# Kernel optimization log

Measured on AMD Instinct MI355X. Metric: run time of the kernel, lower is better.

The kernel has to match this reference:

```python
import jax, jax.numpy as jnp
from jax import lax
import numpy as np

SUB_SAMPLE = 16
NMS_THRESH = 0.7
N_PRE_NMS = 2000
N_POST_NMS = 300
MIN_SIZE = 16.0
SCALE = 1.0
NEG_INF = -1e9


def _anchor_base(base=16.0, ratios=(0.5, 1.0, 2.0), scales=(8.0, 16.0, 32.0)):
    r = np.asarray(ratios, np.float32)[:, None]
    s = np.asarray(scales, np.float32)[None, :]
    h = base * s * np.sqrt(r)
    w = base * s * np.sqrt(1.0 / r)
    ctr = base / 2.0
    ab = np.stack([ctr - h / 2, ctr - w / 2, ctr + h / 2, ctr + w / 2], axis=-1)
    return ab.reshape(-1, 4).astype(np.float32)  # [9,4] (y1,x1,y2,x2)


def _decode(anchors, locs):
    # anchors/locs: [K,4]; loc2bbox
    ah = anchors[:, 2] - anchors[:, 0]
    aw = anchors[:, 3] - anchors[:, 1]
    acy = anchors[:, 0] + 0.5 * ah
    acx = anchors[:, 1] + 0.5 * aw
    dy, dx, dh, dw = locs[:, 0], locs[:, 1], locs[:, 2], locs[:, 3]
    cy = dy * ah + acy
    cx = dx * aw + acx
    h = jnp.exp(dh) * ah
    w = jnp.exp(dw) * aw
    return jnp.stack([cy - 0.5 * h, cx - 0.5 * w, cy + 0.5 * h, cx + 0.5 * w], axis=-1)


def _pairwise_iou(b):
    # b: [P,4] y1x1y2x2
    tl = jnp.maximum(b[:, None, :2], b[None, :, :2])
    br = jnp.minimum(b[:, None, 2:], b[None, :, 2:])
    wh = jnp.clip(br - tl, 0.0)
    inter = wh[..., 0] * wh[..., 1]
    area = (b[:, 2] - b[:, 0]) * (b[:, 3] - b[:, 1])
    return inter / (area[:, None] + area[None, :] - inter + 1e-9)


def _propose(locs_i, fg_i, anchors, img_h, img_w):
    boxes = _decode(anchors, locs_i)
    boxes = jnp.stack([
        jnp.clip(boxes[:, 0], 0.0, img_h), jnp.clip(boxes[:, 1], 0.0, img_w),
        jnp.clip(boxes[:, 2], 0.0, img_h), jnp.clip(boxes[:, 3], 0.0, img_w)], axis=-1)
    hs = boxes[:, 2] - boxes[:, 0]
    ws = boxes[:, 3] - boxes[:, 1]
    ok = (hs >= MIN_SIZE * SCALE) & (ws >= MIN_SIZE * SCALE)
    sc = jnp.where(ok, fg_i, NEG_INF)
    top_sc, order = lax.top_k(sc, N_PRE_NMS)  # sorted desc by score
    b = boxes[order]
    iou = _pairwise_iou(b)
    idx = jnp.arange(N_PRE_NMS)
    sup = (iou > NMS_THRESH) & (idx[None, :] > idx[:, None])  # only suppress lower-scored
    keep0 = top_sc > NEG_INF / 2  # drop min-size-filtered padding

    def body(i, keep):
        return jnp.where(keep[i], keep & ~sup[i], keep)

    keep = lax.fori_loop(0, N_PRE_NMS, body, keep0)
    prio = jnp.where(keep, idx, N_PRE_NMS)
    sel = jnp.argsort(prio)[:N_POST_NMS]  # kept boxes first, score order preserved
    valid = keep[sel]
    rois = jnp.where(valid[:, None], b[sel], 0.0)
    return rois, valid


def setup_inputs() -> dict:
    key = jax.random.key(0)
    ks = jax.random.split(key, 6)
    N, C, Hf, Wf = 8, 512, 64, 64
    std = 0.01  # normal_init(0, 0.01)
    return {
        "x": jax.random.normal(ks[0], (N, C, Hf, Wf), jnp.float32),
        "conv1_w": jax.random.normal(ks[1], (512, 512, 3, 3), jnp.float32) * std,
        "conv1_b": jnp.zeros((512,), jnp.float32),
        "score_w": jax.random.normal(ks[2], (18, 512, 1, 1), jnp.float32) * std,
        "score_b": jnp.zeros((18,), jnp.float32),
        "loc_w": jax.random.normal(ks[3], (36, 512, 1, 1), jnp.float32) * std,
        "loc_b": jnp.zeros((36,), jnp.float32),
        "img_h": 1024,
        "img_w": 1024,
    }


def reference(x, conv1_w, conv1_b, score_w, score_b, loc_w, loc_b, img_h, img_w):
    N, _, Hf, Wf = x.shape
    ab = jnp.asarray(_anchor_base())
    A = ab.shape[0]
    sy = jnp.arange(Hf, dtype=jnp.float32) * SUB_SAMPLE
    sx = jnp.arange(Wf, dtype=jnp.float32) * SUB_SAMPLE
    Y, X = jnp.meshgrid(sy, sx, indexing='ij')
    shifts = jnp.stack([Y, X, Y, X], axis=-1).reshape(-1, 4)
    anchors = (shifts[:, None, :] + ab[None, :, :]).reshape(-1, 4)  # [H*W*A,4]

    hidden = jax.nn.relu(
        lax.conv_general_dilated(x, conv1_w, (1, 1), 'SAME',
                                 dimension_numbers=('NCHW', 'OIHW', 'NCHW'))
        + conv1_b[None, :, None, None])
    scores = jnp.einsum('nchw,oc->nhwo', hidden, score_w[:, :, 0, 0]) + score_b  # [N,H,W,2A]
    locs = jnp.einsum('nchw,oc->nhwo', hidden, loc_w[:, :, 0, 0]) + loc_b        # [N,H,W,4A]

    rpn_locs = locs.reshape(N, -1, 4)
    rpn_scores = scores.reshape(N, -1, 2)
    soft = jax.nn.softmax(scores.reshape(N, Hf, Wf, A, 2), axis=-1)
    rpn_fg = soft[..., 1].reshape(N, -1)

    fh = jnp.float32(img_h)
    fw = jnp.float32(img_w)
    rois, valid = jax.vmap(lambda l, s: _propose(l, s, anchors, fh, fw))(rpn_locs, rpn_fg)
    roi_indices = jnp.repeat(jnp.arange(N, dtype=jnp.int32), N_POST_NMS)
    return rpn_locs, rpn_scores, rois.reshape(-1, 4), roi_indices, anchors
```

## Files before the change

### kernel.cpp

```cpp
#include <hip/hip_runtime.h>
#include <math.h>

typedef unsigned int u32;
typedef unsigned long long u64;

#define NIMG 8
#define CIN 512
#define COUT 512
#define HF 64
#define WF 64
#define NPOS 4096
#define NANCH 36864
#define NPRE 2000
#define NPOST 300
#define SUPW 32

#define OUT_LOCS   0
#define OUT_SCORES 1179648
#define OUT_ROIS   1769472
#define OUT_ROIIDX 1779072
#define OUT_ANCH   1781472

__device__ __forceinline__ u32 fkey(float f) {
  u32 s = __float_as_uint(f);
  return (s & 0x80000000u) ? ~s : (s | 0x80000000u);
}
__device__ __forceinline__ float unkey(u32 u) {
  u32 s = (u & 0x80000000u) ? (u ^ 0x80000000u) : ~u;
  return __uint_as_float(s);
}
__device__ __forceinline__ void anchor_at(int hq, int wq, int a,
                                          float& a0, float& a1, float& a2, float& a3) {
  const float ratios[3] = {0.5f, 1.0f, 2.0f};
  const float scales[3] = {8.0f, 16.0f, 32.0f};
  float r = ratios[a / 3];
  float s = scales[a % 3];
  float hh = __fmul_rn(__fmul_rn(16.0f, s), sqrtf(r));
  float ww = __fmul_rn(__fmul_rn(16.0f, s), sqrtf(1.0f / r));
  float ab0 = __fsub_rn(8.0f, __fmul_rn(0.5f, hh));
  float ab1 = __fsub_rn(8.0f, __fmul_rn(0.5f, ww));
  float ab2 = __fadd_rn(8.0f, __fmul_rn(0.5f, hh));
  float ab3 = __fadd_rn(8.0f, __fmul_rn(0.5f, ww));
  float y = (float)(hq * 16);
  float x = (float)(wq * 16);
  a0 = __fadd_rn(y, ab0);
  a1 = __fadd_rn(x, ab1);
  a2 = __fadd_rn(y, ab2);
  a3 = __fadd_rn(x, ab3);
}
__device__ __forceinline__ u64 shfl_u64(u64 v, int src) {
  u32 lo = (u32)v, hi = (u32)(v >> 32);
  lo = __shfl(lo, src, 64);
  hi = __shfl(hi, src, 64);
  return ((u64)hi << 32) | (u64)lo;
}

__global__ __launch_bounds__(256) void k_transpose_w(const float* __restrict__ w,
                                                     float* __restrict__ wt) {
  int o = blockIdx.x * 256 + threadIdx.x;
  if (o >= COUT * CIN * 9) return;
  int co = o & 511;
  int r = o >> 9;
  int tap = r % 9;
  int ci = r / 9;
  wt[o] = w[((size_t)co * CIN + ci) * 9 + tap];
}

__global__ __launch_bounds__(256) void k_prep_small(const float* __restrict__ sw,
                                                    const float* __restrict__ lw,
                                                    float* __restrict__ wt54,
                                                    float* __restrict__ out) {
  int i = blockIdx.x * 256 + threadIdx.x;
  if (i < 512 * 56) {
    int c = i / 56, o = i % 56;
    float v = 0.0f;
    if (o < 18) v = sw[o * 512 + c];
    else if (o < 54) v = lw[(o - 18) * 512 + c];
    wt54[i] = v;
  }
  if (i < NANCH) {
    int pos = i / 9, a = i % 9;
    float a0, a1, a2, a3;
    anchor_at(pos >> 6, pos & 63, a, a0, a1, a2, a3);
    float* dst = out + OUT_ANCH + (size_t)i * 4;
    dst[0] = a0; dst[1] = a1; dst[2] = a2; dst[3] = a3;
  }
  if (i < NIMG * NPOST) out[OUT_ROIIDX + i] = (float)(i / NPOST);
}

#define CC 8
__global__ __launch_bounds__(256) void k_conv3x3(const float* __restrict__ x,
                                                 const float* __restrict__ wt,
                                                 const float* __restrict__ bias,
                                                 float* __restrict__ hidden) {
  __shared__ float in_lds[4][CC][68];
  __shared__ float w_lds[CC][9][64];
  const int tid = threadIdx.x;
  const int h0 = blockIdx.x * 2;
  const int n = blockIdx.y;
  const int co_t = blockIdx.z * 64;
  const int wq = tid & 15, cq = tid >> 4;
  const int w0 = wq * 4;
  const float* xn = x + (size_t)n * CIN * NPOS;
  float acc[2][4][4] = {};
  for (int ci0 = 0; ci0 < CIN; ci0 += CC) {
    for (int idx = tid; idx < 4 * CC * 66; idx += 256) {
      int wp = idx % 66;
      int r = idx / 66;
      int cc = r % CC, rr = r / CC;
      int hh = h0 - 1 + rr, ww = wp - 1;
      float v = 0.0f;
      if (hh >= 0 && hh < HF && ww >= 0 && ww < WF)
        v = xn[(size_t)(ci0 + cc) * NPOS + hh * WF + ww];
      in_lds[rr][cc][wp] = v;
    }
    for (int idx = tid; idx < CC * 9 * 64; idx += 256) {
      int co = idx & 63;
      int r = idx >> 6;
      int tap = r % 9, cc = r / 9;
      w_lds[cc][tap][co] = wt[((size_t)(ci0 + cc) * 9 + tap) * COUT + co_t + co];
    }
    __syncthreads();
    for (int cc = 0; cc < CC; ++cc) {
      float a[4][6];
      #pragma unroll
      for (int r = 0; r < 4; ++r)
        #pragma unroll
        for (int k = 0; k < 6; ++k)
          a[r][k] = in_lds[r][cc][w0 + k];
      #pragma unroll
      for (int kh = 0; kh < 3; ++kh) {
        #pragma unroll
        for (int kw = 0; kw < 3; ++kw) {
          const float4 b4 = *(const float4*)&w_lds[cc][kh * 3 + kw][cq * 4];
          #pragma unroll
          for (int r = 0; r < 2; ++r) {
            #pragma unroll
            for (int w = 0; w < 4; ++w) {
              float av = a[r + kh][w + kw];
              acc[r][w][0] = fmaf(av, b4.x, acc[r][w][0]);
              acc[r][w][1] = fmaf(av, b4.y, acc[r][w][1]);
              acc[r][w][2] = fmaf(av, b4.z, acc[r][w][2]);
              acc[r][w][3] = fmaf(av, b4.w, acc[r][w][3]);
            }
          }
        }
      }
    }
    __syncthreads();
  }
  #pragma unroll
  for (int c = 0; c < 4; ++c) {
    float b = bias[co_t + cq * 4 + c];
    #pragma unroll
    for (int r = 0; r < 2; ++r) {
      float4 v;
      v.x = fmaxf(acc[r][0][c] + b, 0.0f);
      v.y = fmaxf(acc[r][1][c] + b, 0.0f);
      v.z = fmaxf(acc[r][2][c] + b, 0.0f);
      v.w = fmaxf(acc[r][3][c] + b, 0.0f);
      *(float4*)&hidden[(((size_t)n * COUT + co_t + cq * 4 + c) * HF + h0 + r) * WF + w0] = v;
    }
  }
}

__global__ __launch_bounds__(256) void k_heads(const float* __restrict__ hidden,
                                               const float* __restrict__ wt54,
                                               const float* __restrict__ sb,
                                               const float* __restrict__ lb,
                                               const int* __restrict__ ihp,
                                               const int* __restrict__ iwp,
                                               float* __restrict__ out,
                                               float4* __restrict__ boxes_all,
                                               u64* __restrict__ k64) {
  const int n = blockIdx.y;
  const int hw = blockIdx.x * 256 + threadIdx.x;
  const float* hid = hidden + (size_t)n * CIN * NPOS + hw;
  float acc[54];
  #pragma unroll
  for (int o = 0; o < 54; ++o) acc[o] = 0.0f;
  #pragma unroll 4
  for (int c = 0; c < CIN; ++c) {
    float hv = hid[(size_t)c * NPOS];
    const float* wrow = wt54 + c * 56;
    #pragma unroll
    for (int o = 0; o < 54; ++o) acc[o] = fmaf(hv, wrow[o], acc[o]);
  }
  float sc18[18];
  #pragma unroll
  for (int o = 0; o < 18; ++o) sc18[o] = __fadd_rn(acc[o], sb[o]);
  float lc36[36];
  #pragma unroll
  for (int o = 0; o < 36; ++o) lc36[o] = __fadd_rn(acc[18 + o], lb[o]);
  {
    float* dst = out + OUT_SCORES + ((size_t)n * NPOS + hw) * 18;
    #pragma unroll
    for (int q = 0; q < 9; ++q) *(float2*)&dst[q * 2] = make_float2(sc18[2 * q], sc18[2 * q + 1]);
  }
  {
    float* dst = out + OUT_LOCS + ((size_t)n * NPOS + hw) * 36;
    #pragma unroll
    for (int q = 0; q < 9; ++q)
      *(float4*)&dst[q * 4] = make_float4(lc36[4 * q], lc36[4 * q + 1], lc36[4 * q + 2], lc36[4 * q + 3]);
  }
  const float fh = (float)ihp[0];
  const float fw = (float)iwp[0];
  const int hq = hw >> 6, wq2 = hw & 63;
  #pragma unroll
  for (int a = 0; a < 9; ++a) {
    float a0, a1, a2, a3;
    anchor_at(hq, wq2, a, a0, a1, a2, a3);
    float ah = __fsub_rn(a2, a0), aw = __fsub_rn(a3, a1);
    float acy = __fadd_rn(a0, __fmul_rn(0.5f, ah));
    float acx = __fadd_rn(a1, __fmul_rn(0.5f, aw));
    float dy = lc36[4 * a], dx = lc36[4 * a + 1], dh = lc36[4 * a + 2], dw = lc36[4 * a + 3];
    float cy = __fadd_rn(__fmul_rn(dy, ah), acy);
    float cx = __fadd_rn(__fmul_rn(dx, aw), acx);
    float hh = __fmul_rn(expf(dh), ah);
    float ww = __fmul_rn(expf(dw), aw);
    float y1 = __fsub_rn(cy, __fmul_rn(0.5f, hh));
    float x1 = __fsub_rn(cx, __fmul_rn(0.5f, ww));
    float y2 = __fadd_rn(cy, __fmul_rn(0.5f, hh));
    float x2 = __fadd_rn(cx, __fmul_rn(0.5f, ww));
    y1 = fminf(fmaxf(y1, 0.0f), fh);
    y2 = fminf(fmaxf(y2, 0.0f), fh);
    x1 = fminf(fmaxf(x1, 0.0f), fw);
    x2 = fminf(fmaxf(x2, 0.0f), fw);
    float hs = __fsub_rn(y2, y1), wsz = __fsub_rn(x2, x1);
    bool ok = (hs >= 16.0f) && (wsz >= 16.0f);
    float l0 = sc18[2 * a], l1 = sc18[2 * a + 1];
    float m = fmaxf(l0, l1);
    float e0 = expf(__fsub_rn(l0, m));
    float e1 = expf(__fsub_rn(l1, m));
    float fg = __fdiv_rn(e1, __fadd_rn(e0, e1));
    float sc = ok ? fg : -1000000000.0f;
    int idx = hw * 9 + a;
    boxes_all[(size_t)n * NANCH + idx] = make_float4(y1, x1, y2, x2);
    k64[(size_t)n * NANCH + idx] = ((u64)(~fkey(sc)) << 16) | (u32)idx;
  }
}

__global__ __launch_bounds__(1024) void k_topk(const u64* __restrict__ k64_all,
                                               const float4* __restrict__ boxes_all,
                                               float4* __restrict__ boxes_sorted,
                                               float* __restrict__ sc_sorted) {
  const int b = blockIdx.x;
  const int tid = threadIdx.x;
  const u64* kb = k64_all + (size_t)b * NANCH;
  __shared__ u32 hist[4096];
  __shared__ u32 coarse[1024];
  __shared__ u64 sortbuf[2048];
  __shared__ u32 sh_bucket, sh_before, sh_cnt;
  u64 prefix = 0ull;
  u32 rank = NPRE;
  for (int pass = 0; pass < 4; ++pass) {
    const int shift = 36 - 12 * pass;
    for (int i = tid; i < 4096; i += 1024) hist[i] = 0;
    __syncthreads();
    for (int i = tid; i < NANCH; i += 1024) {
      u64 k = kb[i];
      if ((k >> (shift + 12)) == prefix)
        atomicAdd(&hist[(u32)((k >> shift) & 4095ull)], 1u);
    }
    __syncthreads();
    u32 s = hist[4 * tid] + hist[4 * tid + 1] + hist[4 * tid + 2] + hist[4 * tid + 3];
    coarse[tid] = s;
    __syncthreads();
    for (int off = 1; off < 1024; off <<= 1) {
      u32 v = (tid >= off) ? coarse[tid - off] : 0u;
      __syncthreads();
      coarse[tid] += v;
      __syncthreads();
    }
    u32 lo = (tid == 0) ? 0u : coarse[tid - 1];
    u32 hi = coarse[tid];
    if (lo < rank && rank <= hi) {
      u32 c = lo;
      #pragma unroll
      for (int q = 0; q < 4; ++q) {
        u32 nb = c + hist[4 * tid + q];
        if (c < rank && rank <= nb) { sh_bucket = 4 * tid + q; sh_before = c; break; }
        c = nb;
      }
    }
    __syncthreads();
    prefix = (prefix << 12) | (u64)sh_bucket;
    rank -= sh_before;
    __syncthreads();
  }
  const u64 Kstar = prefix;
  if (tid == 0) sh_cnt = 0;
  __syncthreads();
  for (int i = tid; i < NANCH; i += 1024) {
    u64 k = kb[i];
    if (k <= Kstar) {
      u32 p = atomicAdd(&sh_cnt, 1u);
      if (p < 2048) sortbuf[p] = k;
    }
  }
  __syncthreads();
  u32 cnt = sh_cnt;
  for (int i = tid; i < 2048; i += 1024)
    if (i >= (int)cnt) sortbuf[i] = ~0ull;
  __syncthreads();
  for (int kk = 2; kk <= 2048; kk <<= 1) {
    for (int j = kk >> 1; j > 0; j >>= 1) {
      int i1 = 2 * j * (tid / j) + (tid % j);
      int i2 = i1 + j;
      bool up = ((i1 & kk) == 0);
      u64 va = sortbuf[i1], vb = sortbuf[i2];
      if ((va > vb) == up) { sortbuf[i1] = vb; sortbuf[i2] = va; }
      __syncthreads();
    }
  }
  for (int i = tid; i < NPRE; i += 1024) {
    u64 k = sortbuf[i];
    u32 idx = (u32)(k & 0xFFFFull);
    boxes_sorted[(size_t)b * NPRE + i] = boxes_all[(size_t)b * NANCH + idx];
    sc_sorted[(size_t)b * NPRE + i] = unkey(~(u32)(k >> 16));
  }
}

__global__ __launch_bounds__(64) void k_supmask(const float4* __restrict__ boxes_sorted,
                                                u64* __restrict__ sup) {
  const int b = blockIdx.z;
  const int i = blockIdx.x * 64 + threadIdx.x;
  const int j0 = blockIdx.y * 64;
  __shared__ float4 bj[64];
  int jg = j0 + threadIdx.x;
  bj[threadIdx.x] = (jg < NPRE) ? boxes_sorted[(size_t)b * NPRE + jg] : make_float4(0, 0, 0, 0);
  __syncthreads();
  if (i >= NPRE) return;
  float4 bi = boxes_sorted[(size_t)b * NPRE + i];
  float ai = __fmul_rn(__fsub_rn(bi.z, bi.x), __fsub_rn(bi.w, bi.y));
  u64 m = 0;
  for (int q = 0; q < 64; ++q) {
    int j = j0 + q;
    float4 bb = bj[q];
    float ty = fmaxf(bi.x, bb.x);
    float tx = fmaxf(bi.y, bb.y);
    float by = fminf(bi.z, bb.z);
    float bx = fminf(bi.w, bb.w);
    float ih2 = fmaxf(__fsub_rn(by, ty), 0.0f);
    float iw2 = fmaxf(__fsub_rn(bx, tx), 0.0f);
    float inter = __fmul_rn(ih2, iw2);
    float aj = __fmul_rn(__fsub_rn(bb.z, bb.x), __fsub_rn(bb.w, bb.y));
    float den = __fadd_rn(__fsub_rn(__fadd_rn(ai, aj), inter), 1e-9f);
    float iou = __fdiv_rn(inter, den);
    if (iou > 0.7f && j > i && j < NPRE) m |= (1ull << q);
  }
  sup[((size_t)b * NPRE + i) * SUPW + blockIdx.y] = m;
}

__global__ __launch_bounds__(64) void k_nms(const u64* __restrict__ sup,
                                            const float* __restrict__ sc_sorted,
                                            const float4* __restrict__ boxes_sorted,
                                            float* __restrict__ rois) {
  const int b = blockIdx.x;
  const int lane = threadIdx.x;
  __shared__ float sc[NPRE];
  for (int i = lane; i < NPRE; i += 64) sc[i] = sc_sorted[(size_t)b * NPRE + i];
  __syncthreads();
  const u64* supb = sup + (size_t)b * NPRE * SUPW;
  const float* bs = (const float*)(boxes_sorted + (size_t)b * NPRE);
  float* rb = rois + (size_t)b * NPOST * 4;
  u64 removed = 0ull;
  int kc = 0;
  for (int i = 0; i < NPRE; ++i) {
    int w = i >> 6;
    u64 rw = shfl_u64(removed, w);
    bool kept = (((rw >> (i & 63)) & 1ull) == 0ull) && (sc[i] > -5.0e8f);
    if (kept) {
      if (lane < 4) rb[(size_t)kc * 4 + lane] = bs[(size_t)i * 4 + lane];
      ++kc;
      if (kc >= NPOST) break;
      if (lane < 32) removed |= supb[(size_t)i * SUPW + lane];
    }
  }
  for (int z = lane; z < (NPOST - kc) * 4; z += 64) rb[(size_t)kc * 4 + z] = 0.0f;
}

extern "C" void kernel_launch(void* const* d_in, const int* in_sizes, int n_in,
                              void* d_out, int out_size, void* d_ws, size_t ws_size,
                              hipStream_t stream) {
  const float* x  = (const float*)d_in[0];
  const float* w1 = (const float*)d_in[1];
  const float* b1 = (const float*)d_in[2];
  const float* sw = (const float*)d_in[3];
  const float* sb = (const float*)d_in[4];
  const float* lw = (const float*)d_in[5];
  const float* lb = (const float*)d_in[6];
  const int* ih   = (const int*)d_in[7];
  const int* iw   = (const int*)d_in[8];
  float* out = (float*)d_out;
  char* ws = (char*)d_ws;

  float* hidden       = (float*)(ws + 0);
  float* wt           = (float*)(ws + 67108864ull);
  float* wt54         = (float*)(ws + 76546048ull);
  float4* boxes_all   = (float4*)(ws + 67108864ull);
  u64*   k64          = (u64*)  (ws + 71827456ull);
  float4* boxes_sorted= (float4*)(ws + 0);
  float* sc_sorted    = (float*)(ws + 262144ull);
  u64*   sup          = (u64*)  (ws + 327680ull);
  (void)in_sizes; (void)n_in; (void)out_size; (void)ws_size;

  k_transpose_w<<<9216, 256, 0, stream>>>(w1, wt);
  k_prep_small<<<144, 256, 0, stream>>>(sw, lw, wt54, out);
  k_conv3x3<<<dim3(32, 8, 8), 256, 0, stream>>>(x, wt, b1, hidden);
  k_heads<<<dim3(16, 8), 256, 0, stream>>>(hidden, wt54, sb, lb, ih, iw, out, boxes_all, k64);
  k_topk<<<8, 1024, 0, stream>>>(k64, boxes_all, boxes_sorted, sc_sorted);
  k_supmask<<<dim3(32, 32, 8), 64, 0, stream>>>(boxes_sorted, sup);
  k_nms<<<8, 64, 0, stream>>>(sup, sc_sorted, boxes_sorted, out + OUT_ROIS);
}
```

Baseline: 2.263 ms.

## Retile 3x3 conv into 32x32 spatial tiles with 16x8 register blocking

```diff
diff --git a/kernel.cpp b/kernel.cpp
--- a/kernel.cpp
+++ b/kernel.cpp
@@ -55,17 +55,6 @@
   return ((u64)hi << 32) | (u64)lo;
 }
 
-__global__ __launch_bounds__(256) void k_transpose_w(const float* __restrict__ w,
-                                                     float* __restrict__ wt) {
-  int o = blockIdx.x * 256 + threadIdx.x;
-  if (o >= COUT * CIN * 9) return;
-  int co = o & 511;
-  int r = o >> 9;
-  int tap = r % 9;
-  int ci = r / 9;
-  wt[o] = w[((size_t)co * CIN + ci) * 9 + tap];
-}
-
 __global__ __launch_bounds__(256) void k_prep_small(const float* __restrict__ sw,
                                                     const float* __restrict__ lw,
                                                     float* __restrict__ wt54,
@@ -88,60 +77,79 @@
   if (i < NIMG * NPOST) out[OUT_ROIIDX + i] = (float)(i / NPOST);
 }
 
-#define CC 8
-__global__ __launch_bounds__(256) void k_conv3x3(const float* __restrict__ x,
-                                                 const float* __restrict__ wt,
-                                                 const float* __restrict__ bias,
-                                                 float* __restrict__ hidden) {
-  __shared__ float in_lds[4][CC][68];
-  __shared__ float w_lds[CC][9][64];
+__global__ __launch_bounds__(256) void k_transpose_w(const float* __restrict__ w,
+                                                     float* __restrict__ wt) {
+  int o = blockIdx.x * 256 + threadIdx.x;
+  if (o >= COUT * CIN * 9) return;
+  int co = o & 511;
+  int r = o >> 9;
+  int tap = r % 9;
+  int ci = r / 9;
+  wt[o] = w[((size_t)co * CIN + ci) * 9 + tap];
+}
+
+#define TCI 4
+__global__ __launch_bounds__(256, 2) void k_conv_fast(const float* __restrict__ x,
+                                                      const float* __restrict__ wt,
+                                                      const float* __restrict__ bias,
+                                                      float* __restrict__ hidden) {
+  __shared__ float in_lds[TCI][34][36];
+  __shared__ float w_lds[TCI][9][32];
   const int tid = threadIdx.x;
-  const int h0 = blockIdx.x * 2;
-  const int n = blockIdx.y;
-  const int co_t = blockIdx.z * 64;
-  const int wq = tid & 15, cq = tid >> 4;
-  const int w0 = wq * 4;
+  const int n  = blockIdx.x >> 2;
+  const int h0 = ((blockIdx.x >> 1) & 1) * 32;
+  const int w0 = (blockIdx.x & 1) * 32;
+  const int co0 = blockIdx.y * 32;
+  const int pix = tid & 63, cg = tid >> 6;
+  const int py = (pix >> 3) * 4, px = (pix & 7) * 4;
   const float* xn = x + (size_t)n * CIN * NPOS;
-  float acc[2][4][4] = {};
-  for (int ci0 = 0; ci0 < CIN; ci0 += CC) {
-    for (int idx = tid; idx < 4 * CC * 66; idx += 256) {
-      int wp = idx % 66;
-      int r = idx / 66;
-      int cc = r % CC, rr = r / CC;
-      int hh = h0 - 1 + rr, ww = wp - 1;
+  float acc[16][8] = {};
+
+  for (int ci0 = 0; ci0 < CIN; ci0 += TCI) {
+    for (int idx = tid; idx < TCI * 34 * 34; idx += 256) {
+      int w = idx % 34;
+      int r = (idx / 34) % 34;
+      int c = idx / (34 * 34);
+      int gh = h0 + r - 1, gw = w0 + w - 1;
       float v = 0.0f;
-      if (hh >= 0 && hh < HF && ww >= 0 && ww < WF)
-        v = xn[(size_t)(ci0 + cc) * NPOS + hh * WF + ww];
-      in_lds[rr][cc][wp] = v;
-    }
-    for (int idx = tid; idx < CC * 9 * 64; idx += 256) {
-      int co = idx & 63;
-      int r = idx >> 6;
-      int tap = r % 9, cc = r / 9;
-      w_lds[cc][tap][co] = wt[((size_t)(ci0 + cc) * 9 + tap) * COUT + co_t + co];
-    }
-    __syncthreads();
-    for (int cc = 0; cc < CC; ++cc) {
-      float a[4][6];
+      if (gh >= 0 && gh < HF && gw >= 0 && gw < WF)
+        v = xn[(size_t)(ci0 + c) * NPOS + gh * WF + gw];
+      in_lds[c][r][w] = v;
+    }
+    for (int idx = tid; idx < TCI * 9 * 32; idx += 256) {
+      int co = idx & 31;
+      int tap = (idx >> 5) % 9;
+      int c = idx / (9 * 32);
+      w_lds[c][tap][co] = wt[((size_t)(ci0 + c) * 9 + tap) * COUT + co0 + co];
+    }
+    __syncthreads();
+    #pragma unroll 1
+    for (int c = 0; c < TCI; ++c) {
+      float p[6][6];
       #pragma unroll
-      for (int r = 0; r < 4; ++r)
+      for (int r = 0; r < 6; ++r)
         #pragma unroll
-        for (int k = 0; k < 6; ++k)
-          a[r][k] = in_lds[r][cc][w0 + k];
+        for (int q = 0; q < 6; ++q)
+          p[r][q] = in_lds[c][py + r][px + q];
       #pragma unroll
       for (int kh = 0; kh < 3; ++kh) {
         #pragma unroll
         for (int kw = 0; kw < 3; ++kw) {
-          const float4 b4 = *(const float4*)&w_lds[cc][kh * 3 + kw][cq * 4];
+          const float4 wa = *(const float4*)&w_lds[c][kh * 3 + kw][cg * 8];
+          const float4 wb = *(const float4*)&w_lds[c][kh * 3 + kw][cg * 8 + 4];
           #pragma unroll
-          for (int r = 0; r < 2; ++r) {
+          for (int r = 0; r < 4; ++r) {
             #pragma unroll
-            for (int w = 0; w < 4; ++w) {
-              float av = a[r + kh][w + kw];
-              acc[r][w][0] = fmaf(av, b4.x, acc[r][w][0]);
-              acc[r][w][1] = fmaf(av, b4.y, acc[r][w][1]);
-              acc[r][w][2] = fmaf(av, b4.z, acc[r][w][2]);
-              acc[r][w][3] = fmaf(av, b4.w, acc[r][w][3]);
+            for (int q = 0; q < 4; ++q) {
+              const float a = p[r + kh][q + kw];
+              acc[r * 4 + q][0] = fmaf(a, wa.x, acc[r * 4 + q][0]);
+              acc[r * 4 + q][1] = fmaf(a, wa.y, acc[r * 4 + q][1]);
+              acc[r * 4 + q][2] = fmaf(a, wa.z, acc[r * 4 + q][2]);
+              acc[r * 4 + q][3] = fmaf(a, wa.w, acc[r * 4 + q][3]);
+              acc[r * 4 + q][4] = fmaf(a, wb.x, acc[r * 4 + q][4]);
+              acc[r * 4 + q][5] = fmaf(a, wb.y, acc[r * 4 + q][5]);
+              acc[r * 4 + q][6] = fmaf(a, wb.z, acc[r * 4 + q][6]);
+              acc[r * 4 + q][7] = fmaf(a, wb.w, acc[r * 4 + q][7]);
             }
           }
         }
@@ -150,16 +158,17 @@
     __syncthreads();
   }
   #pragma unroll
-  for (int c = 0; c < 4; ++c) {
-    float b = bias[co_t + cq * 4 + c];
+  for (int co = 0; co < 8; ++co) {
+    const float b = bias[co0 + cg * 8 + co];
+    float* dst = hidden + ((size_t)(n * COUT + co0 + cg * 8 + co)) * NPOS;
     #pragma unroll
-    for (int r = 0; r < 2; ++r) {
+    for (int r = 0; r < 4; ++r) {
       float4 v;
-      v.x = fmaxf(acc[r][0][c] + b, 0.0f);
-      v.y = fmaxf(acc[r][1][c] + b, 0.0f);
-      v.z = fmaxf(acc[r][2][c] + b, 0.0f);
-      v.w = fmaxf(acc[r][3][c] + b, 0.0f);
-      *(float4*)&hidden[(((size_t)n * COUT + co_t + cq * 4 + c) * HF + h0 + r) * WF + w0] = v;
+      v.x = fmaxf(acc[r * 4 + 0][co] + b, 0.0f);
+      v.y = fmaxf(acc[r * 4 + 1][co] + b, 0.0f);
+      v.z = fmaxf(acc[r * 4 + 2][co] + b, 0.0f);
+      v.w = fmaxf(acc[r * 4 + 3][co] + b, 0.0f);
+      *(float4*)&dst[(h0 + py + r) * WF + (w0 + px)] = v;
     }
   }
 }
@@ -394,6 +403,7 @@
   const int* iw   = (const int*)d_in[8];
   float* out = (float*)d_out;
   char* ws = (char*)d_ws;
+  (void)in_sizes; (void)n_in; (void)out_size; (void)ws_size;
 
   float* hidden       = (float*)(ws + 0);
   float* wt           = (float*)(ws + 67108864ull);
@@ -403,11 +413,10 @@
   float4* boxes_sorted= (float4*)(ws + 0);
   float* sc_sorted    = (float*)(ws + 262144ull);
   u64*   sup          = (u64*)  (ws + 327680ull);
-  (void)in_sizes; (void)n_in; (void)out_size; (void)ws_size;
 
   k_transpose_w<<<9216, 256, 0, stream>>>(w1, wt);
   k_prep_small<<<144, 256, 0, stream>>>(sw, lw, wt54, out);
-  k_conv3x3<<<dim3(32, 8, 8), 256, 0, stream>>>(x, wt, b1, hidden);
+  k_conv_fast<<<dim3(32, 16), 256, 0, stream>>>(x, wt, b1, hidden);
   k_heads<<<dim3(16, 8), 256, 0, stream>>>(hidden, wt54, sb, lb, ih, iw, out, boxes_all, k64);
   k_topk<<<8, 1024, 0, stream>>>(k64, boxes_all, boxes_sorted, sc_sorted);
   k_supmask<<<dim3(32, 32, 8), 64, 0, stream>>>(boxes_sorted, sup);
```

Result: slower. 2.538 ms (+12.2%).
